# Kernel optimization log

Measured on AMD Instinct MI355X. Metric: run time of the kernel, lower is better.

The kernel has to match this reference:

```python
import jax, jax.numpy as jnp
import numpy as np

SCALE = 0.1
TEMP = 1.0
LN_EPS = 1e-6
NORM_EPS = 1e-12  # torch F.normalize eps


def setup_inputs() -> dict:
    key = jax.random.key(0)
    k1, = jax.random.split(key, 1)
    B, N, D = 8, 2048, 256
    x = jax.random.normal(k1, (B, N, D), dtype=jnp.float32)
    ln_gamma = jnp.ones((D,), dtype=jnp.float32)
    ln_beta = jnp.zeros((D,), dtype=jnp.float32)
    return {"x": x, "ln_gamma": ln_gamma, "ln_beta": ln_beta}


def reference(x, ln_gamma, ln_beta):
    # L2-normalize along feature dim (torch F.normalize, dim=2)
    norm = jnp.sqrt(jnp.sum(x * x, axis=2, keepdims=True))
    xn = x / jnp.maximum(norm, NORM_EPS)
    # self-similarity: [B, N, N]
    sim = jnp.einsum('bnd,bmd->bnm', xn, xn) / TEMP
    # dual_norm: row softmax + column softmax
    sim = jax.nn.softmax(sim, axis=2) + jax.nn.softmax(sim, axis=1)
    x_neg = jnp.einsum('bnm,bmd->bnd', sim, x)
    x = x - SCALE * x_neg
    # LayerNorm(dim), eps=1e-6
    mu = jnp.mean(x, axis=-1, keepdims=True)
    var = jnp.mean((x - mu) ** 2, axis=-1, keepdims=True)
    xhat = (x - mu) * jax.lax.rsqrt(var + LN_EPS)
    return xhat * ln_gamma + ln_beta
```

## Files before the change

### kernel.cpp

```cpp
#include <hip/hip_runtime.h>

namespace {
constexpr int Bv = 8;
constexpr int Nv = 2048;
constexpr int Dv = 256;
constexpr float SCALE = 0.1f;
constexpr float PSCALE = 256.0f;
constexpr float OSC = SCALE / PSCALE;
constexpr float LN_EPS = 1e-6f;
constexpr float NORM_EPS = 1e-12f;
}

typedef unsigned char u8;
typedef unsigned int u32;
typedef __attribute__((ext_vector_type(4))) float f32x4;

__device__ __forceinline__ void gll16(const void* g, void* l) {
    __builtin_amdgcn_global_load_lds(
        (__attribute__((address_space(1))) void*)(uintptr_t)g,
        (__attribute__((address_space(3))) void*)(uintptr_t)l, 16, 0, 0);
}
__device__ __forceinline__ u32 pk4(float a, float b, float c, float d) {
    u32 w = __builtin_amdgcn_cvt_pk_fp8_f32(a, b, 0, false);
    return __builtin_amdgcn_cvt_pk_fp8_f32(c, d, w, true);
}

__global__ __launch_bounds__(512) void k_prepT(const float* __restrict__ x,
                                               u8* __restrict__ xn8,
                                               u8* __restrict__ xT8) {
    __shared__ u8 lt[64][272];
    const int b = blockIdx.x >> 5;
    const int n0 = (blockIdx.x & 31) * 64;
    const int t = threadIdx.x;
    const int r = t >> 3, c0 = (t & 7) * 32;
    const float* xr = x + ((size_t)b * Nv + n0 + r) * Dv + c0;
    float4 v[8];
    float ss = 0.f;
#pragma unroll
    for (int i = 0; i < 8; ++i) {
        v[i] = ((const float4*)xr)[i];
        ss += v[i].x * v[i].x + v[i].y * v[i].y + v[i].z * v[i].z + v[i].w * v[i].w;
    }
#pragma unroll
    for (int m = 1; m < 8; m <<= 1) ss += __shfl_xor(ss, m, 64);
    const float inv = 1.0f / fmaxf(sqrtf(ss), NORM_EPS);
    u32 wn[8];
#pragma unroll
    for (int i = 0; i < 8; ++i) {
        wn[i] = pk4(v[i].x * inv, v[i].y * inv, v[i].z * inv, v[i].w * inv);
        *(u32*)&lt[r][c0 + i * 4] = pk4(v[i].x, v[i].y, v[i].z, v[i].w);
    }
    {
        uint4 o0 = {wn[0], wn[1], wn[2], wn[3]};
        uint4 o1 = {wn[4], wn[5], wn[6], wn[7]};
        u8* xnr = xn8 + ((size_t)b * Nv + n0 + r) * Dv + c0;
        *(uint4*)xnr = o0;
        *(uint4*)(xnr + 16) = o1;
    }
    __syncthreads();
    {
        const int d = t >> 1, h = t & 1;
        u32 w2[8];
#pragma unroll
        for (int q = 0; q < 8; ++q) {
            const int nb = h * 32 + q * 4;
            w2[q] = (u32)lt[nb][d] | ((u32)lt[nb + 1][d] << 8) |
                    ((u32)lt[nb + 2][d] << 16) | ((u32)lt[nb + 3][d] << 24);
        }
        uint4 p0 = {w2[0], w2[1], w2[2], w2[3]};
        uint4 p1 = {w2[4], w2[5], w2[6], w2[7]};
        u8* xtr = xT8 + ((size_t)b * Dv + d) * Nv + n0 + h * 32;
        *(uint4*)xtr = p0;
        *(uint4*)(xtr + 16) = p1;
    }
}

__global__ __launch_bounds__(512, 4) void k_gemm1(const u8* __restrict__ xn8,
                                                  u8* __restrict__ E,
                                                  float* __restrict__ rl) {
    __shared__ u8 Bs[2][128 * 256];
    __shared__ u8 eS[2][128 * 40];
    __shared__ float red[32][4];
    const int wg = blockIdx.x;
    const int b = wg & 7, bi = wg >> 3;
    const int t = threadIdx.x;
    const int wave = t >> 6, lane = t & 63;
    const int wr = wave >> 2, wc = wave & 3;
    const int l15 = lane & 15, kl = lane >> 4;
    const u8* xb = xn8 + (size_t)b * (Nv * Dv);

    auto stageB = [&](int buf, int ch) {
#pragma unroll
        for (int c = 0; c < 4; ++c) {
            const int row = wave * 16 + c * 4 + (lane >> 4);
            const int slot = (lane & 15) ^ (row & 15);
            gll16(xb + (size_t)(ch * 128 + row) * Dv + slot * 16,
                  Bs[buf] + wave * 4096 + c * 1024);
        }
    };
    auto bfrag = [&](const u8* base, int row, int kk) -> long {
        const int slot = kk * 2 + (kl >> 1);
        return *(const long*)(base + row * 256 +
                              ((slot ^ (row & 15)) << 4) + ((kl & 1) << 3));
    };

    const int ch0 = bi >> 2;
    stageB(0, ch0);
    __syncthreads();
    long af[8];
    {
        const int arow = (bi & 3) * 32 + wr * 16 + l15;
#pragma unroll
        for (int kk = 0; kk < 8; ++kk) af[kk] = bfrag(Bs[0], arow, kk);
    }
    float rs[4] = {0.f, 0.f, 0.f, 0.f};
    u8* Eb = E + (size_t)b * Nv * Nv;
    int cur = 0;
    for (int cc = 0; cc < 16; ++cc) {
        const int ch = (ch0 + cc) & 15;
        if (cc < 15) stageB(cur ^ 1, (ch0 + cc + 1) & 15);
        f32x4 acc[2] = {};
#pragma unroll
        for (int kk = 0; kk < 8; ++kk) {
            const long b0 = bfrag(Bs[cur], wc * 32 + l15, kk);
            const long b1 = bfrag(Bs[cur], wc * 32 + 16 + l15, kk);
            acc[0] = __builtin_amdgcn_mfma_f32_16x16x32_fp8_fp8(af[kk], b0, acc[0], 0, 0, 0);
            acc[1] = __builtin_amdgcn_mfma_f32_16x16x32_fp8_fp8(af[kk], b1, acc[1], 0, 0, 0);
        }
#pragma unroll
        for (int j = 0; j < 2; ++j) {
            const int col = wc * 32 + j * 16 + l15;
            const float e0 = __expf(acc[j][0] - 1.0f);
            const float e1 = __expf(acc[j][1] - 1.0f);
            const float e2 = __expf(acc[j][2] - 1.0f);
            const float e3 = __expf(acc[j][3] - 1.0f);
            rs[0] += e0; rs[1] += e1; rs[2] += e2; rs[3] += e3;
            *(u32*)&eS[cur][col * 40 + wr * 16 + kl * 4] = pk4(e0, e1, e2, e3);
        }
        __syncthreads();
        {
            const int c = t >> 2, sg = t & 3;
            *(uint2*)&Eb[(size_t)(ch * 128 + c) * Nv + bi * 32 + sg * 8] =
                *(const uint2*)&eS[cur][c * 40 + sg * 8];
        }
        cur ^= 1;
    }
#pragma unroll
    for (int r = 0; r < 4; ++r) {
        float v = rs[r];
#pragma unroll
        for (int m = 1; m < 16; m <<= 1) v += __shfl_xor(v, m, 64);
        if (l15 == 0) red[wr * 16 + kl * 4 + r][wc] = v;
    }
    __syncthreads();
    if (t < 32)
        rl[b * Nv + bi * 32 + t] =
            PSCALE * __builtin_amdgcn_rcpf(red[t][0] + red[t][1] + red[t][2] + red[t][3]);
}

__global__ __launch_bounds__(512) void k_gemm2ln(const u8* __restrict__ E,
                                                 const float* __restrict__ rl,
                                                 const u8* __restrict__ xT8,
                                                 const float* __restrict__ x,
                                                 const float* __restrict__ gamma,
                                                 const float* __restrict__ beta,
                                                 float* __restrict__ out) {
    __shared__ u8 Bs[2][256 * 128];
    __shared__ u8 Ps[2][32 * 136];
    __shared__ float red[32][8][2];
    const int wg = blockIdx.x;
    const int swz = (wg & 7) * 64 + (wg >> 3);
    const int b = swz >> 6, bi = swz & 63;
    const int t = threadIdx.x;
    const int wave = t >> 6, lane = t & 63;
    const int l15 = lane & 15, kl = lane >> 4;
    const int srow = t >> 4, s16 = t & 15;
    const float* rlb = rl + (size_t)b * Nv;
    const u8* Erow = E + ((size_t)b * Nv + bi * 32 + srow) * Nv + s16 * 8;
    const u8* xtb = xT8 + (size_t)b * 524288;

    auto issueB = [&](int buf, int kt) {
#pragma unroll
        for (int c = 0; c < 4; ++c) {
            const int row = c * 64 + wave * 8 + (lane >> 3);
            const int slot = (lane & 7) ^ (row & 7);
            gll16(xtb + (size_t)row * Nv + kt * 128 + slot * 16,
                  (char*)Bs[buf] + c * 8192 + wave * 1024);
        }
    };
    auto bfragB = [&](const u8* base, int d, int kk) -> long {
        const int s = kk * 2 + (kl >> 1);
        return *(const long*)(base + d * 128 + ((s ^ (d & 7)) << 4) + ((kl & 1) << 3));
    };
    auto afrag = [&](const u8* base, int row, int kk) -> long {
        return *(const long*)(base + row * 136 + kk * 32 + kl * 8);
    };

    const float linv_n = rlb[bi * 32 + srow];
    auto wstore = [&](u8* pbuf, uint2 ev, float4 ra, float4 rb) {
        const u32 o0 = pk4(__builtin_amdgcn_cvt_f32_fp8(ev.x, 0) * (linv_n + ra.x),
                           __builtin_amdgcn_cvt_f32_fp8(ev.x, 1) * (linv_n + ra.y),
                           __builtin_amdgcn_cvt_f32_fp8(ev.x, 2) * (linv_n + ra.z),
                           __builtin_amdgcn_cvt_f32_fp8(ev.x, 3) * (linv_n + ra.w));
        const u32 o1 = pk4(__builtin_amdgcn_cvt_f32_fp8(ev.y, 0) * (linv_n + rb.x),
                           __builtin_amdgcn_cvt_f32_fp8(ev.y, 1) * (linv_n + rb.y),
                           __builtin_amdgcn_cvt_f32_fp8(ev.y, 2) * (linv_n + rb.z),
                           __builtin_amdgcn_cvt_f32_fp8(ev.y, 3) * (linv_n + rb.w));
        uint2 o = {o0, o1};
        *(uint2*)(pbuf + srow * 136 + s16 * 8) = o;
    };

    issueB(0, 0);
    uint2 evB = *(const uint2*)(Erow);
    float4 raB = *(const float4*)&rlb[s16 * 8];
    float4 rbB = *(const float4*)&rlb[s16 * 8 + 4];
    wstore(Ps[0], evB, raB, rbB);
    evB = *(const uint2*)(Erow + 128);
    uint2 evC = *(const uint2*)(Erow + 256);
    raB = *(const float4*)&rlb[128 + s16 * 8];
    rbB = *(const float4*)&rlb[128 + s16 * 8 + 4];
    __syncthreads();

    f32x4 acc[2][2] = {};
    int cur = 0;
    for (int kt = 0; kt < 16; ++kt) {
        if (kt < 15) issueB(cur ^ 1, kt + 1);
#pragma unroll
        for (int kk = 0; kk < 4; ++kk) {
            const long a0 = afrag(Ps[cur], l15, kk);
            const long a1 = afrag(Ps[cur], 16 + l15, kk);
            const long b0 = bfragB(Bs[cur], wave * 32 + l15, kk);
            const long b1 = bfragB(Bs[cur], wave * 32 + 16 + l15, kk);
            acc[0][0] = __builtin_amdgcn_mfma_f32_16x16x32_fp8_fp8(a0, b0, acc[0][0], 0, 0, 0);
            acc[0][1] = __builtin_amdgcn_mfma_f32_16x16x32_fp8_fp8(a0, b1, acc[0][1], 0, 0, 0);
            acc[1][0] = __builtin_amdgcn_mfma_f32_16x16x32_fp8_fp8(a1, b0, acc[1][0], 0, 0, 0);
            acc[1][1] = __builtin_amdgcn_mfma_f32_16x16x32_fp8_fp8(a1, b1, acc[1][1], 0, 0, 0);
        }
        if (kt < 15) {
            wstore(Ps[cur ^ 1], evB, raB, rbB);
            evB = evC;
            if (kt < 14) {
                evC = *(const uint2*)(Erow + (kt + 2) * 128);
                raB = *(const float4*)&rlb[(kt + 1) * 128 + s16 * 8];
                rbB = *(const float4*)&rlb[(kt + 1) * 128 + s16 * 8 + 4];
            }
        }
        __syncthreads();
        cur ^= 1;
    }
    const float* xb = x + ((size_t)b * Nv + bi * 32) * Dv;
    float tv[2][2][4];
#pragma unroll
    for (int i = 0; i < 2; ++i) {
#pragma unroll
        for (int r = 0; r < 4; ++r) {
            const int rr = i * 16 + kl * 4 + r;
            float s1 = 0.f, s2 = 0.f;
#pragma unroll
            for (int j = 0; j < 2; ++j) {
                const int cc = wave * 32 + j * 16 + l15;
                const float v = xb[(size_t)rr * Dv + cc] - OSC * acc[i][j][r];
                tv[i][j][r] = v;
                s1 += v; s2 += v * v;
            }
#pragma unroll
            for (int m = 1; m < 16; m <<= 1) {
                s1 += __shfl_xor(s1, m, 64);
                s2 += __shfl_xor(s2, m, 64);
            }
            if (l15 == 0) { red[rr][wave][0] = s1; red[rr][wave][1] = s2; }
        }
    }
    __syncthreads();
#pragma unroll
    for (int i = 0; i < 2; ++i) {
#pragma unroll
        for (int r = 0; r < 4; ++r) {
            const int rr = i * 16 + kl * 4 + r;
            float s1 = 0.f, s2 = 0.f;
#pragma unroll
            for (int w = 0; w < 8; ++w) { s1 += red[rr][w][0]; s2 += red[rr][w][1]; }
            const float mu = s1 * (1.0f / Dv);
            const float var = s2 * (1.0f / Dv) - mu * mu;
            const float rstd = rsqrtf(var + LN_EPS);
#pragma unroll
            for (int j = 0; j < 2; ++j) {
                const int cc = wave * 32 + j * 16 + l15;
                out[((size_t)b * Nv + bi * 32 + rr) * Dv + cc] =
                    (tv[i][j][r] - mu) * rstd * gamma[cc] + beta[cc];
            }
        }
    }
}

extern "C" void kernel_launch(void* const* d_in, const int* in_sizes, int n_in,
                              void* d_out, int out_size, void* d_ws, size_t ws_size,
                              hipStream_t stream) {
    const float* x = (const float*)d_in[0];
    const float* gamma = (const float*)d_in[1];
    const float* beta = (const float*)d_in[2];
    float* out = (float*)d_out;
    char* ws = (char*)d_ws;
    u8* xn8 = (u8*)ws;
    u8* xT8 = (u8*)(ws + 4194304);
    float* rl = (float*)(ws + 8388608);
    u8* E = (u8*)(ws + 8454144);

    k_prepT<<<Bv * (Nv / 64), 512, 0, stream>>>(x, xn8, xT8);
    k_gemm1<<<Bv * (Nv / 32), 512, 0, stream>>>(xn8, E, rl);
    k_gemm2ln<<<Bv * (Nv / 32), 512, 0, stream>>>(E, rl, xT8, x, gamma, beta, out);
}
```

Before: 66.11 us.

## Replace syncthreads with manual vmcnt waits and deeper prefetch in both GEMM kernels

Both GEMM loops now use explicit s_waitcnt vmcnt/lgkmcnt plus raw s_barrier in place of __syncthreads. This lets global-to-LDS loads for the next two stages stay in flight while the current stage computes. MFMA sections are wrapped in s_setprio to favour matrix issue. The vmcnt counts must exactly match the outstanding load counts, so any miscount risks races or reading stale LDS data.

Measured after the change: 66.74 us. About the same (+1.0%).

```diff
diff --git a/kernel.cpp b/kernel.cpp
--- a/kernel.cpp
+++ b/kernel.cpp
@@ -14,6 +14,11 @@
 typedef unsigned char u8;
 typedef unsigned int u32;
 typedef __attribute__((ext_vector_type(4))) float f32x4;
+
+#define SBAR()   asm volatile("s_barrier" ::: "memory")
+#define WAITV(N) asm volatile("s_waitcnt vmcnt(" #N ")" ::: "memory")
+#define WAITL()  asm volatile("s_waitcnt lgkmcnt(0)" ::: "memory")
+#define CFENCE() asm volatile("" ::: "memory")
 
 __device__ __forceinline__ void gll16(const void* g, void* l) {
     __builtin_amdgcn_global_load_lds(
@@ -88,6 +93,8 @@
     const int wr = wave >> 2, wc = wave & 3;
     const int l15 = lane & 15, kl = lane >> 4;
     const u8* xb = xn8 + (size_t)b * (Nv * Dv);
+    u8* Eb = E + (size_t)b * Nv * Nv;
+    const int sc = t >> 2, sg = t & 3;
 
     auto stageB = [&](int buf, int ch) {
 #pragma unroll
@@ -106,7 +113,9 @@
 
     const int ch0 = bi >> 2;
     stageB(0, ch0);
-    __syncthreads();
+    CFENCE();
+    stageB(1, (ch0 + 1) & 15);
+    WAITV(4); SBAR();
     long af[8];
     {
         const int arow = (bi & 3) * 32 + wr * 16 + l15;
@@ -114,12 +123,10 @@
         for (int kk = 0; kk < 8; ++kk) af[kk] = bfrag(Bs[0], arow, kk);
     }
     float rs[4] = {0.f, 0.f, 0.f, 0.f};
-    u8* Eb = E + (size_t)b * Nv * Nv;
-    int cur = 0;
-    for (int cc = 0; cc < 16; ++cc) {
-        const int ch = (ch0 + cc) & 15;
-        if (cc < 15) stageB(cur ^ 1, (ch0 + cc + 1) & 15);
+
+    auto phaseA = [&](int cur) {
         f32x4 acc[2] = {};
+        __builtin_amdgcn_s_setprio(1);
 #pragma unroll
         for (int kk = 0; kk < 8; ++kk) {
             const long b0 = bfrag(Bs[cur], wc * 32 + l15, kk);
@@ -127,6 +134,7 @@
             acc[0] = __builtin_amdgcn_mfma_f32_16x16x32_fp8_fp8(af[kk], b0, acc[0], 0, 0, 0);
             acc[1] = __builtin_amdgcn_mfma_f32_16x16x32_fp8_fp8(af[kk], b1, acc[1], 0, 0, 0);
         }
+        __builtin_amdgcn_s_setprio(0);
 #pragma unroll
         for (int j = 0; j < 2; ++j) {
             const int col = wc * 32 + j * 16 + l15;
@@ -137,14 +145,27 @@
             rs[0] += e0; rs[1] += e1; rs[2] += e2; rs[3] += e3;
             *(u32*)&eS[cur][col * 40 + wr * 16 + kl * 4] = pk4(e0, e1, e2, e3);
         }
-        __syncthreads();
-        {
-            const int c = t >> 2, sg = t & 3;
-            *(uint2*)&Eb[(size_t)(ch * 128 + c) * Nv + bi * 32 + sg * 8] =
-                *(const uint2*)&eS[cur][c * 40 + sg * 8];
-        }
-        cur ^= 1;
-    }
+    };
+    auto estore = [&](int cur, int ch) {
+        *(uint2*)&Eb[(size_t)(ch * 128 + sc) * Nv + bi * 32 + sg * 8] =
+            *(const uint2*)&eS[cur][sc * 40 + sg * 8];
+    };
+
+    for (int cc = 0; cc < 14; ++cc) {
+        const int cur = cc & 1;
+        phaseA(cur);
+        WAITL(); SBAR();
+        estore(cur, (ch0 + cc) & 15);
+        stageB(cur, (ch0 + cc + 2) & 15);
+        WAITV(5); SBAR();
+    }
+    phaseA(0);
+    WAITL(); SBAR();
+    estore(0, (ch0 + 14) & 15);
+    WAITV(1); SBAR();
+    phaseA(1);
+    WAITL(); SBAR();
+    estore(1, (ch0 + 15) & 15);
 #pragma unroll
     for (int r = 0; r < 4; ++r) {
         float v = rs[r];
@@ -209,22 +230,15 @@
         uint2 o = {o0, o1};
         *(uint2*)(pbuf + srow * 136 + s16 * 8) = o;
     };
-
-    issueB(0, 0);
-    uint2 evB = *(const uint2*)(Erow);
-    float4 raB = *(const float4*)&rlb[s16 * 8];
-    float4 rbB = *(const float4*)&rlb[s16 * 8 + 4];
-    wstore(Ps[0], evB, raB, rbB);
-    evB = *(const uint2*)(Erow + 128);
-    uint2 evC = *(const uint2*)(Erow + 256);
-    raB = *(const float4*)&rlb[128 + s16 * 8];
-    rbB = *(const float4*)&rlb[128 + s16 * 8 + 4];
-    __syncthreads();
+    auto loadgrp = [&](int nk, uint2& ev, float4& ra, float4& rb) {
+        ev = *(const uint2*)(Erow + nk * 128);
+        ra = *(const float4*)&rlb[nk * 128 + s16 * 8];
+        rb = *(const float4*)&rlb[nk * 128 + s16 * 8 + 4];
+    };
 
     f32x4 acc[2][2] = {};
-    int cur = 0;
-    for (int kt = 0; kt < 16; ++kt) {
-        if (kt < 15) issueB(cur ^ 1, kt + 1);
+    auto phaseA = [&](int cur) {
+        __builtin_amdgcn_s_setprio(1);
 #pragma unroll
         for (int kk = 0; kk < 4; ++kk) {
             const long a0 = afrag(Ps[cur], l15, kk);
@@ -236,18 +250,40 @@
             acc[1][0] = __builtin_amdgcn_mfma_f32_16x16x32_fp8_fp8(a1, b0, acc[1][0], 0, 0, 0);
             acc[1][1] = __builtin_amdgcn_mfma_f32_16x16x32_fp8_fp8(a1, b1, acc[1][1], 0, 0, 0);
         }
-        if (kt < 15) {
-            wstore(Ps[cur ^ 1], evB, raB, rbB);
-            evB = evC;
-            if (kt < 14) {
-                evC = *(const uint2*)(Erow + (kt + 2) * 128);
-                raB = *(const float4*)&rlb[(kt + 1) * 128 + s16 * 8];
-                rbB = *(const float4*)&rlb[(kt + 1) * 128 + s16 * 8 + 4];
-            }
-        }
-        __syncthreads();
-        cur ^= 1;
-    }
+        __builtin_amdgcn_s_setprio(0);
+    };
+
+    uint2 evA, evB2;
+    float4 raA, rbA, raB2, rbB2;
+    loadgrp(0, evA, raA, rbA);
+    issueB(0, 0);
+    CFENCE();
+    loadgrp(1, evB2, raB2, rbB2);
+    issueB(1, 1);
+    CFENCE();
+    wstore(Ps[0], evA, raA, rbA);
+    WAITL(); WAITV(7); SBAR();
+
+    for (int kt2 = 0; kt2 < 7; ++kt2) {
+        phaseA(0);
+        wstore(Ps[1], evB2, raB2, rbB2);
+        WAITL(); SBAR();
+        loadgrp(2 * kt2 + 2, evA, raA, rbA);
+        issueB(0, 2 * kt2 + 2);
+        WAITV(7); SBAR();
+        phaseA(1);
+        wstore(Ps[0], evA, raA, rbA);
+        WAITL(); SBAR();
+        loadgrp(2 * kt2 + 3, evB2, raB2, rbB2);
+        issueB(1, 2 * kt2 + 3);
+        WAITV(7); SBAR();
+    }
+    phaseA(0);
+    wstore(Ps[1], evB2, raB2, rbB2);
+    WAITL(); SBAR();
+    WAITV(0); SBAR();
+    phaseA(1);
+
     const float* xb = x + ((size_t)b * Nv + bi * 32) * Dv;
     float tv[2][2][4];
 #pragma unroll
```

## Double row tile to 64 in both GEMM kernels and restructure staging

Applied to the files above, without the earlier changes.

Both GEMM kernels now process 64 rows per workgroup instead of 32, halving the grid to 256 blocks. Each wave computes more MFMA tiles per loaded B fragment, so the same B chunk is reused across twice the rows and fewer passes over xn8 and xT8 are needed. The pipeline changes from prefetching the next buffer before compute to prefetching two stages ahead after compute. The P tile in the second kernel loses its double buffering, and the LayerNorm reduction scratch now reuses that shared buffer. The trade-off is half as many blocks on a 256-CU part and more registers per thread, which may lower occupancy and latency hiding.

New measurement: 77.21 us. 1.17x slower.

```diff
diff --git a/kernel.cpp b/kernel.cpp
--- a/kernel.cpp
+++ b/kernel.cpp
@@ -75,19 +75,20 @@
     }
 }
 
-__global__ __launch_bounds__(512, 4) void k_gemm1(const u8* __restrict__ xn8,
-                                                  u8* __restrict__ E,
-                                                  float* __restrict__ rl) {
+__global__ __launch_bounds__(512) void k_gemm1(const u8* __restrict__ xn8,
+                                               u8* __restrict__ E,
+                                               float* __restrict__ rl) {
     __shared__ u8 Bs[2][128 * 256];
-    __shared__ u8 eS[2][128 * 40];
-    __shared__ float red[32][4];
+    __shared__ u8 eS[128 * 80];
+    __shared__ float red[64][4];
     const int wg = blockIdx.x;
     const int b = wg & 7, bi = wg >> 3;
     const int t = threadIdx.x;
     const int wave = t >> 6, lane = t & 63;
-    const int wr = wave >> 2, wc = wave & 3;
+    const int wrp = wave >> 2, wc = wave & 3;
     const int l15 = lane & 15, kl = lane >> 4;
     const u8* xb = xn8 + (size_t)b * (Nv * Dv);
+    u8* Eb = E + (size_t)b * Nv * Nv;
 
     auto stageB = [&](int buf, int ch) {
 #pragma unroll
@@ -104,57 +105,70 @@
                               ((slot ^ (row & 15)) << 4) + ((kl & 1) << 3));
     };
 
-    const int ch0 = bi >> 2;
+    const int ch0 = bi >> 1;
     stageB(0, ch0);
     __syncthreads();
-    long af[8];
+    long af[2][8];
     {
-        const int arow = (bi & 3) * 32 + wr * 16 + l15;
-#pragma unroll
-        for (int kk = 0; kk < 8; ++kk) af[kk] = bfrag(Bs[0], arow, kk);
-    }
-    float rs[4] = {0.f, 0.f, 0.f, 0.f};
-    u8* Eb = E + (size_t)b * Nv * Nv;
-    int cur = 0;
+#pragma unroll
+        for (int i = 0; i < 2; ++i) {
+            const int arow = (bi & 1) * 64 + wrp * 32 + i * 16 + l15;
+#pragma unroll
+            for (int kk = 0; kk < 8; ++kk) af[i][kk] = bfrag(Bs[0], arow, kk);
+        }
+    }
+    stageB(1, (ch0 + 1) & 15);
+    __syncthreads();
+
+    float rs[2][4] = {};
     for (int cc = 0; cc < 16; ++cc) {
         const int ch = (ch0 + cc) & 15;
-        if (cc < 15) stageB(cur ^ 1, (ch0 + cc + 1) & 15);
-        f32x4 acc[2] = {};
+        const int cur = cc & 1;
+        f32x4 acc[2][2] = {};
 #pragma unroll
         for (int kk = 0; kk < 8; ++kk) {
             const long b0 = bfrag(Bs[cur], wc * 32 + l15, kk);
             const long b1 = bfrag(Bs[cur], wc * 32 + 16 + l15, kk);
-            acc[0] = __builtin_amdgcn_mfma_f32_16x16x32_fp8_fp8(af[kk], b0, acc[0], 0, 0, 0);
-            acc[1] = __builtin_amdgcn_mfma_f32_16x16x32_fp8_fp8(af[kk], b1, acc[1], 0, 0, 0);
-        }
-#pragma unroll
-        for (int j = 0; j < 2; ++j) {
-            const int col = wc * 32 + j * 16 + l15;
-            const float e0 = __expf(acc[j][0] - 1.0f);
-            const float e1 = __expf(acc[j][1] - 1.0f);
-            const float e2 = __expf(acc[j][2] - 1.0f);
-            const float e3 = __expf(acc[j][3] - 1.0f);
-            rs[0] += e0; rs[1] += e1; rs[2] += e2; rs[3] += e3;
-            *(u32*)&eS[cur][col * 40 + wr * 16 + kl * 4] = pk4(e0, e1, e2, e3);
+#pragma unroll
+            for (int i = 0; i < 2; ++i) {
+                acc[i][0] = __builtin_amdgcn_mfma_f32_16x16x32_fp8_fp8(af[i][kk], b0, acc[i][0], 0, 0, 0);
+                acc[i][1] = __builtin_amdgcn_mfma_f32_16x16x32_fp8_fp8(af[i][kk], b1, acc[i][1], 0, 0, 0);
+            }
+        }
+#pragma unroll
+        for (int i = 0; i < 2; ++i) {
+#pragma unroll
+            for (int j = 0; j < 2; ++j) {
+                const int col = wc * 32 + j * 16 + l15;
+                const float e0 = __expf(acc[i][j][0] - 1.0f);
+                const float e1 = __expf(acc[i][j][1] - 1.0f);
+                const float e2 = __expf(acc[i][j][2] - 1.0f);
+                const float e3 = __expf(acc[i][j][3] - 1.0f);
+                rs[i][0] += e0; rs[i][1] += e1; rs[i][2] += e2; rs[i][3] += e3;
+                *(u32*)&eS[col * 80 + wrp * 32 + i * 16 + kl * 4] = pk4(e0, e1, e2, e3);
+            }
         }
         __syncthreads();
         {
-            const int c = t >> 2, sg = t & 3;
-            *(uint2*)&Eb[(size_t)(ch * 128 + c) * Nv + bi * 32 + sg * 8] =
-                *(const uint2*)&eS[cur][c * 40 + sg * 8];
-        }
-        cur ^= 1;
-    }
-#pragma unroll
-    for (int r = 0; r < 4; ++r) {
-        float v = rs[r];
-#pragma unroll
-        for (int m = 1; m < 16; m <<= 1) v += __shfl_xor(v, m, 64);
-        if (l15 == 0) red[wr * 16 + kl * 4 + r][wc] = v;
-    }
-    __syncthreads();
-    if (t < 32)
-        rl[b * Nv + bi * 32 + t] =
+            const int m = t >> 2, q = t & 3;
+            *(uint4*)&Eb[(size_t)(ch * 128 + m) * Nv + bi * 64 + q * 16] =
+                *(const uint4*)&eS[m * 80 + q * 16];
+        }
+        if (cc < 14) stageB(cur, (ch0 + cc + 2) & 15);
+        __syncthreads();
+    }
+#pragma unroll
+    for (int i = 0; i < 2; ++i)
+#pragma unroll
+        for (int r = 0; r < 4; ++r) {
+            float v = rs[i][r];
+#pragma unroll
+            for (int m = 1; m < 16; m <<= 1) v += __shfl_xor(v, m, 64);
+            if (l15 == 0) red[wrp * 32 + i * 16 + kl * 4 + r][wc] = v;
+        }
+    __syncthreads();
+    if (t < 64)
+        rl[b * Nv + bi * 64 + t] =
             PSCALE * __builtin_amdgcn_rcpf(red[t][0] + red[t][1] + red[t][2] + red[t][3]);
 }
 
@@ -166,17 +180,17 @@
                                                  const float* __restrict__ beta,
                                                  float* __restrict__ out) {
     __shared__ u8 Bs[2][256 * 128];
-    __shared__ u8 Ps[2][32 * 136];
-    __shared__ float red[32][8][2];
+    __shared__ u8 Ps[64 * 144];
     const int wg = blockIdx.x;
-    const int swz = (wg & 7) * 64 + (wg >> 3);
-    const int b = swz >> 6, bi = swz & 63;
+    const int swz = (wg & 7) * 32 + (wg >> 3);
+    const int b = swz >> 5, bi = swz & 31;
     const int t = threadIdx.x;
     const int wave = t >> 6, lane = t & 63;
+    const int wrp = wave >> 2, wcol = wave & 3;
     const int l15 = lane & 15, kl = lane >> 4;
-    const int srow = t >> 4, s16 = t & 15;
+    const int srow = t >> 3, s8 = t & 7;
     const float* rlb = rl + (size_t)b * Nv;
-    const u8* Erow = E + ((size_t)b * Nv + bi * 32 + srow) * Nv + s16 * 8;
+    const u8* Erow = E + ((size_t)b * Nv + bi * 64 + srow) * Nv + s8 * 16;
     const u8* xtb = xT8 + (size_t)b * 524288;
 
     auto issueB = [&](int buf, int kt) {
@@ -192,73 +206,87 @@
         const int s = kk * 2 + (kl >> 1);
         return *(const long*)(base + d * 128 + ((s ^ (d & 7)) << 4) + ((kl & 1) << 3));
     };
-    auto afrag = [&](const u8* base, int row, int kk) -> long {
-        return *(const long*)(base + row * 136 + kk * 32 + kl * 8);
-    };
-
-    const float linv_n = rlb[bi * 32 + srow];
-    auto wstore = [&](u8* pbuf, uint2 ev, float4 ra, float4 rb) {
-        const u32 o0 = pk4(__builtin_amdgcn_cvt_f32_fp8(ev.x, 0) * (linv_n + ra.x),
-                           __builtin_amdgcn_cvt_f32_fp8(ev.x, 1) * (linv_n + ra.y),
-                           __builtin_amdgcn_cvt_f32_fp8(ev.x, 2) * (linv_n + ra.z),
-                           __builtin_amdgcn_cvt_f32_fp8(ev.x, 3) * (linv_n + ra.w));
-        const u32 o1 = pk4(__builtin_amdgcn_cvt_f32_fp8(ev.y, 0) * (linv_n + rb.x),
-                           __builtin_amdgcn_cvt_f32_fp8(ev.y, 1) * (linv_n + rb.y),
-                           __builtin_amdgcn_cvt_f32_fp8(ev.y, 2) * (linv_n + rb.z),
-                           __builtin_amdgcn_cvt_f32_fp8(ev.y, 3) * (linv_n + rb.w));
-        uint2 o = {o0, o1};
-        *(uint2*)(pbuf + srow * 136 + s16 * 8) = o;
+
+    const float linv_n = rlb[bi * 64 + srow];
+    auto wstore = [&](uint4 ev, float4 r0, float4 r1, float4 r2, float4 r3) {
+        const u32 o0 = pk4(__builtin_amdgcn_cvt_f32_fp8(ev.x, 0) * (linv_n + r0.x),
+                           __builtin_amdgcn_cvt_f32_fp8(ev.x, 1) * (linv_n + r0.y),
+                           __builtin_amdgcn_cvt_f32_fp8(ev.x, 2) * (linv_n + r0.z),
+                           __builtin_amdgcn_cvt_f32_fp8(ev.x, 3) * (linv_n + r0.w));
+        const u32 o1 = pk4(__builtin_amdgcn_cvt_f32_fp8(ev.y, 0) * (linv_n + r1.x),
+                           __builtin_amdgcn_cvt_f32_fp8(ev.y, 1) * (linv_n + r1.y),
+                           __builtin_amdgcn_cvt_f32_fp8(ev.y, 2) * (linv_n + r1.z),
+                           __builtin_amdgcn_cvt_f32_fp8(ev.y, 3) * (linv_n + r1.w));
+        const u32 o2 = pk4(__builtin_amdgcn_cvt_f32_fp8(ev.z, 0) * (linv_n + r2.x),
+                           __builtin_amdgcn_cvt_f32_fp8(ev.z, 1) * (linv_n + r2.y),
+                           __builtin_amdgcn_cvt_f32_fp8(ev.z, 2) * (linv_n + r2.z),
+                           __builtin_amdgcn_cvt_f32_fp8(ev.z, 3) * (linv_n + r2.w));
+        const u32 o3 = pk4(__builtin_amdgcn_cvt_f32_fp8(ev.w, 0) * (linv_n + r3.x),
+                           __builtin_amdgcn_cvt_f32_fp8(ev.w, 1) * (linv_n + r3.y),
+                           __builtin_amdgcn_cvt_f32_fp8(ev.w, 2) * (linv_n + r3.z),
+                           __builtin_amdgcn_cvt_f32_fp8(ev.w, 3) * (linv_n + r3.w));
+        uint4 o = {o0, o1, o2, o3};
+        *(uint4*)&Ps[srow * 144 + s8 * 16] = o;
     };
 
     issueB(0, 0);
-    uint2 evB = *(const uint2*)(Erow);
-    float4 raB = *(const float4*)&rlb[s16 * 8];
-    float4 rbB = *(const float4*)&rlb[s16 * 8 + 4];
-    wstore(Ps[0], evB, raB, rbB);
-    evB = *(const uint2*)(Erow + 128);
-    uint2 evC = *(const uint2*)(Erow + 256);
-    raB = *(const float4*)&rlb[128 + s16 * 8];
-    rbB = *(const float4*)&rlb[128 + s16 * 8 + 4];
-    __syncthreads();
-
-    f32x4 acc[2][2] = {};
-    int cur = 0;
+    uint4 ev = *(const uint4*)(Erow);
+    float4 q0 = *(const float4*)&rlb[s8 * 16];
+    float4 q1 = *(const float4*)&rlb[s8 * 16 + 4];
+    float4 q2 = *(const float4*)&rlb[s8 * 16 + 8];
+    float4 q3 = *(const float4*)&rlb[s8 * 16 + 12];
+    __syncthreads();
+    wstore(ev, q0, q1, q2, q3);
+    issueB(1, 1);
+    ev = *(const uint4*)(Erow + 128);
+    q0 = *(const float4*)&rlb[128 + s8 * 16];
+    q1 = *(const float4*)&rlb[128 + s8 * 16 + 4];
+    q2 = *(const float4*)&rlb[128 + s8 * 16 + 8];
+    q3 = *(const float4*)&rlb[128 + s8 * 16 + 12];
+    __syncthreads();
+
+    f32x4 acc[2][4] = {};
     for (int kt = 0; kt < 16; ++kt) {
-        if (kt < 15) issueB(cur ^ 1, kt + 1);
+        const u8* bs = Bs[kt & 1];
 #pragma unroll
         for (int kk = 0; kk < 4; ++kk) {
-            const long a0 = afrag(Ps[cur], l15, kk);
-            const long a1 = afrag(Ps[cur], 16 + l15, kk);
-            const long b0 = bfragB(Bs[cur], wave * 32 + l15, kk);
-            const long b1 = bfragB(Bs[cur], wave * 32 + 16 + l15, kk);
-            acc[0][0] = __builtin_amdgcn_mfma_f32_16x16x32_fp8_fp8(a0, b0, acc[0][0], 0, 0, 0);
-            acc[0][1] = __builtin_amdgcn_mfma_f32_16x16x32_fp8_fp8(a0, b1, acc[0][1], 0, 0, 0);
-            acc[1][0] = __builtin_amdgcn_mfma_f32_16x16x32_fp8_fp8(a1, b0, acc[1][0], 0, 0, 0);
-            acc[1][1] = __builtin_amdgcn_mfma_f32_16x16x32_fp8_fp8(a1, b1, acc[1][1], 0, 0, 0);
-        }
+            const long a0 = *(const long*)&Ps[(wrp * 32 + l15) * 144 + kk * 32 + kl * 8];
+            const long a1 = *(const long*)&Ps[(wrp * 32 + 16 + l15) * 144 + kk * 32 + kl * 8];
+#pragma unroll
+            for (int j = 0; j < 4; ++j) {
+                const long bj = bfragB(bs, wcol * 64 + j * 16 + l15, kk);
+                acc[0][j] = __builtin_amdgcn_mfma_f32_16x16x32_fp8_fp8(a0, bj, acc[0][j], 0, 0, 0);
+                acc[1][j] = __builtin_amdgcn_mfma_f32_16x16x32_fp8_fp8(a1, bj, acc[1][j], 0, 0, 0);
+            }
+        }
+        __syncthreads();
         if (kt < 15) {
-            wstore(Ps[cur ^ 1], evB, raB, rbB);
-            evB = evC;
+            wstore(ev, q0, q1, q2, q3);
             if (kt < 14) {
-                evC = *(const uint2*)(Erow + (kt + 2) * 128);
-                raB = *(const float4*)&rlb[(kt + 1) * 128 + s16 * 8];
-                rbB = *(const float4*)&rlb[(kt + 1) * 128 + s16 * 8 + 4];
-            }
-        }
-        __syncthreads();
-        cur ^= 1;
-    }
-    const float* xb = x + ((size_t)b * Nv + bi * 32) * Dv;
-    float tv[2][2][4];
+                issueB(kt & 1, kt + 2);
+                const int k2 = (kt + 2) * 128;
+                ev = *(const uint4*)(Erow + k2);
+                q0 = *(const float4*)&rlb[k2 + s8 * 16];
+                q1 = *(const float4*)&rlb[k2 + s8 * 16 + 4];
+                q2 = *(const float4*)&rlb[k2 + s8 * 16 + 8];
+                q3 = *(const float4*)&rlb[k2 + s8 * 16 + 12];
+            }
+            __syncthreads();
+        }
+    }
+    float (*red)[4][2] = (float (*)[4][2])(void*)Ps;
+    __syncthreads();
+    const float* xb = x + ((size_t)b * Nv + bi * 64) * Dv;
+    float tv[2][4][4];
 #pragma unroll
     for (int i = 0; i < 2; ++i) {
 #pragma unroll
         for (int r = 0; r < 4; ++r) {
-            const int rr = i * 16 + kl * 4 + r;
+            const int rr = wrp * 32 + i * 16 + kl * 4 + r;
             float s1 = 0.f, s2 = 0.f;
 #pragma unroll
-            for (int j = 0; j < 2; ++j) {
-                const int cc = wave * 32 + j * 16 + l15;
+            for (int j = 0; j < 4; ++j) {
+                const int cc = wcol * 64 + j * 16 + l15;
                 const float v = xb[(size_t)rr * Dv + cc] - OSC * acc[i][j][r];
                 tv[i][j][r] = v;
                 s1 += v; s2 += v * v;
@@ -268,7 +296,7 @@
                 s1 += __shfl_xor(s1, m, 64);
                 s2 += __shfl_xor(s2, m, 64);
             }
-            if (l15 == 0) { red[rr][wave][0] = s1; red[rr][wave][1] = s2; }
+            if (l15 == 0) { red[rr][wcol][0] = s1; red[rr][wcol][1] = s2; }
         }
     }
     __syncthreads();
@@ -276,17 +304,16 @@
     for (int i = 0; i < 2; ++i) {
 #pragma unroll
         for (int r = 0; r < 4; ++r) {
-            const int rr = i * 16 + kl * 4 + r;
-            float s1 = 0.f, s2 = 0.f;
-#pragma unroll
-            for (int w = 0; w < 8; ++w) { s1 += red[rr][w][0]; s2 += red[rr][w][1]; }
+            const int rr = wrp * 32 + i * 16 + kl * 4 + r;
+            const float s1 = red[rr][0][0] + red[rr][1][0] + red[rr][2][0] + red[rr][3][0];
+            const float s2 = red[rr][0][1] + red[rr][1][1] + red[rr][2][1] + red[rr][3][1];
             const float mu = s1 * (1.0f / Dv);
             const float var = s2 * (1.0f / Dv) - mu * mu;
             const float rstd = rsqrtf(var + LN_EPS);
 #pragma unroll
-            for (int j = 0; j < 2; ++j) {
-                const int cc = wave * 32 + j * 16 + l15;
-                out[((size_t)b * Nv + bi * 32 + rr) * Dv + cc] =
+            for (int j = 0; j < 4; ++j) {
+                const int cc = wcol * 64 + j * 16 + l15;
+                out[((size_t)b * Nv + bi * 64 + rr) * Dv + cc] =
                     (tv[i][j][r] - mu) * rstd * gamma[cc] + beta[cc];
             }
         }
@@ -307,6 +334,6 @@
     u8* E = (u8*)(ws + 8454144);
 
     k_prepT<<<Bv * (Nv / 64), 512, 0, stream>>>(x, xn8, xT8);
-    k_gemm1<<<Bv * (Nv / 32), 512, 0, stream>>>(xn8, E, rl);
-    k_gemm2ln<<<Bv * (Nv / 32), 512, 0, stream>>>(E, rl, xT8, x, gamma, beta, out);
-}
+    k_gemm1<<<Bv * (Nv / 64), 512, 0, stream>>>(xn8, E, rl);
+    k_gemm2ln<<<Bv * (Nv / 64), 512, 0, stream>>>(E, rl, xT8, x, gamma, beta, out);
+}
```

## Enlarge K/N chunks to 256 and switch both GEMMs to single-buffered LDS

Applied to the files above, without the earlier changes.

Both GEMM kernels now stage 256-row (or 256-column) chunks in one LDS buffer instead of double-buffered 128-wide chunks. Each iteration does twice the MFMA work, and the loop has half as many iterations and barriers. E stores and loads also widen to 16-byte vectors. The cost is that global-to-LDS loads are no longer overlapped with compute, since staging happens between two barriers after the compute phase. The min-blocks-per-CU hint is also dropped from gemm1, which may change occupancy.

After: 71.20 us. +7.7%, slower.

```diff
diff --git a/kernel.cpp b/kernel.cpp
--- a/kernel.cpp
+++ b/kernel.cpp
@@ -75,11 +75,11 @@
     }
 }
 
-__global__ __launch_bounds__(512, 4) void k_gemm1(const u8* __restrict__ xn8,
-                                                  u8* __restrict__ E,
-                                                  float* __restrict__ rl) {
-    __shared__ u8 Bs[2][128 * 256];
-    __shared__ u8 eS[2][128 * 40];
+__global__ __launch_bounds__(512) void k_gemm1(const u8* __restrict__ xn8,
+                                               u8* __restrict__ E,
+                                               float* __restrict__ rl) {
+    __shared__ u8 Bs[256 * 256];
+    __shared__ u8 eS[256 * 40];
     __shared__ float red[32][4];
     const int wg = blockIdx.x;
     const int b = wg & 7, bi = wg >> 3;
@@ -88,62 +88,62 @@
     const int wr = wave >> 2, wc = wave & 3;
     const int l15 = lane & 15, kl = lane >> 4;
     const u8* xb = xn8 + (size_t)b * (Nv * Dv);
-
-    auto stageB = [&](int buf, int ch) {
-#pragma unroll
-        for (int c = 0; c < 4; ++c) {
-            const int row = wave * 16 + c * 4 + (lane >> 4);
+    u8* Eb = E + (size_t)b * Nv * Nv;
+
+    auto stage = [&](int ch) {
+#pragma unroll
+        for (int c = 0; c < 8; ++c) {
+            const int row = wave * 32 + c * 4 + (lane >> 4);
             const int slot = (lane & 15) ^ (row & 15);
-            gll16(xb + (size_t)(ch * 128 + row) * Dv + slot * 16,
-                  Bs[buf] + wave * 4096 + c * 1024);
-        }
-    };
-    auto bfrag = [&](const u8* base, int row, int kk) -> long {
+            gll16(xb + (size_t)(ch * 256 + row) * Dv + slot * 16,
+                  Bs + wave * 8192 + c * 1024);
+        }
+    };
+    auto bfrag = [&](int row, int kk) -> long {
         const int slot = kk * 2 + (kl >> 1);
-        return *(const long*)(base + row * 256 +
+        return *(const long*)(Bs + row * 256 +
                               ((slot ^ (row & 15)) << 4) + ((kl & 1) << 3));
     };
 
-    const int ch0 = bi >> 2;
-    stageB(0, ch0);
+    const int ch0 = bi >> 3;
+    stage(ch0);
     __syncthreads();
     long af[8];
     {
-        const int arow = (bi & 3) * 32 + wr * 16 + l15;
-#pragma unroll
-        for (int kk = 0; kk < 8; ++kk) af[kk] = bfrag(Bs[0], arow, kk);
+        const int arow = (bi & 7) * 32 + wr * 16 + l15;
+#pragma unroll
+        for (int kk = 0; kk < 8; ++kk) af[kk] = bfrag(arow, kk);
     }
     float rs[4] = {0.f, 0.f, 0.f, 0.f};
-    u8* Eb = E + (size_t)b * Nv * Nv;
-    int cur = 0;
-    for (int cc = 0; cc < 16; ++cc) {
-        const int ch = (ch0 + cc) & 15;
-        if (cc < 15) stageB(cur ^ 1, (ch0 + cc + 1) & 15);
-        f32x4 acc[2] = {};
+    for (int cc = 0; cc < 8; ++cc) {
+        const int ch = (ch0 + cc) & 7;
+        f32x4 acc[4] = {};
 #pragma unroll
         for (int kk = 0; kk < 8; ++kk) {
-            const long b0 = bfrag(Bs[cur], wc * 32 + l15, kk);
-            const long b1 = bfrag(Bs[cur], wc * 32 + 16 + l15, kk);
-            acc[0] = __builtin_amdgcn_mfma_f32_16x16x32_fp8_fp8(af[kk], b0, acc[0], 0, 0, 0);
-            acc[1] = __builtin_amdgcn_mfma_f32_16x16x32_fp8_fp8(af[kk], b1, acc[1], 0, 0, 0);
-        }
-#pragma unroll
-        for (int j = 0; j < 2; ++j) {
-            const int col = wc * 32 + j * 16 + l15;
+#pragma unroll
+            for (int j = 0; j < 4; ++j) {
+                const long bj = bfrag(wc * 64 + j * 16 + l15, kk);
+                acc[j] = __builtin_amdgcn_mfma_f32_16x16x32_fp8_fp8(af[kk], bj, acc[j], 0, 0, 0);
+            }
+        }
+#pragma unroll
+        for (int j = 0; j < 4; ++j) {
+            const int col = wc * 64 + j * 16 + l15;
             const float e0 = __expf(acc[j][0] - 1.0f);
             const float e1 = __expf(acc[j][1] - 1.0f);
             const float e2 = __expf(acc[j][2] - 1.0f);
             const float e3 = __expf(acc[j][3] - 1.0f);
             rs[0] += e0; rs[1] += e1; rs[2] += e2; rs[3] += e3;
-            *(u32*)&eS[cur][col * 40 + wr * 16 + kl * 4] = pk4(e0, e1, e2, e3);
+            *(u32*)&eS[col * 40 + wr * 16 + kl * 4] = pk4(e0, e1, e2, e3);
         }
         __syncthreads();
         {
-            const int c = t >> 2, sg = t & 3;
-            *(uint2*)&Eb[(size_t)(ch * 128 + c) * Nv + bi * 32 + sg * 8] =
-                *(const uint2*)&eS[cur][c * 40 + sg * 8];
-        }
-        cur ^= 1;
+            const int c2 = t >> 1, half = t & 1;
+            *(uint4*)&Eb[(size_t)(ch * 256 + c2) * Nv + bi * 32 + half * 16] =
+                *(const uint4*)&eS[c2 * 40 + half * 16];
+        }
+        if (cc < 7) stage((ch0 + cc + 1) & 7);
+        __syncthreads();
     }
 #pragma unroll
     for (int r = 0; r < 4; ++r) {
@@ -165,8 +165,8 @@
                                                  const float* __restrict__ gamma,
                                                  const float* __restrict__ beta,
                                                  float* __restrict__ out) {
-    __shared__ u8 Bs[2][256 * 128];
-    __shared__ u8 Ps[2][32 * 136];
+    __shared__ u8 Bs[256 * 256];
+    __shared__ u8 Ps[32 * 264];
     __shared__ float red[32][8][2];
     const int wg = blockIdx.x;
     const int swz = (wg & 7) * 64 + (wg >> 3);
@@ -176,77 +176,93 @@
     const int l15 = lane & 15, kl = lane >> 4;
     const int srow = t >> 4, s16 = t & 15;
     const float* rlb = rl + (size_t)b * Nv;
-    const u8* Erow = E + ((size_t)b * Nv + bi * 32 + srow) * Nv + s16 * 8;
+    const u8* Erow = E + ((size_t)b * Nv + bi * 32 + srow) * Nv + s16 * 16;
     const u8* xtb = xT8 + (size_t)b * 524288;
 
-    auto issueB = [&](int buf, int kt) {
-#pragma unroll
-        for (int c = 0; c < 4; ++c) {
-            const int row = c * 64 + wave * 8 + (lane >> 3);
-            const int slot = (lane & 7) ^ (row & 7);
-            gll16(xtb + (size_t)row * Nv + kt * 128 + slot * 16,
-                  (char*)Bs[buf] + c * 8192 + wave * 1024);
-        }
-    };
-    auto bfragB = [&](const u8* base, int d, int kk) -> long {
-        const int s = kk * 2 + (kl >> 1);
-        return *(const long*)(base + d * 128 + ((s ^ (d & 7)) << 4) + ((kl & 1) << 3));
-    };
-    auto afrag = [&](const u8* base, int row, int kk) -> long {
-        return *(const long*)(base + row * 136 + kk * 32 + kl * 8);
+    auto stage = [&](int kt) {
+#pragma unroll
+        for (int c = 0; c < 8; ++c) {
+            const int row = wave * 32 + c * 4 + (lane >> 4);
+            const int slot = (lane & 15) ^ (row & 15);
+            gll16(xtb + (size_t)row * Nv + kt * 256 + slot * 16,
+                  Bs + wave * 8192 + c * 1024);
+        }
+    };
+    auto bfragB = [&](int d, int kk) -> long {
+        const int slot = kk * 2 + (kl >> 1);
+        return *(const long*)(Bs + d * 256 +
+                              ((slot ^ (d & 15)) << 4) + ((kl & 1) << 3));
     };
 
     const float linv_n = rlb[bi * 32 + srow];
-    auto wstore = [&](u8* pbuf, uint2 ev, float4 ra, float4 rb) {
-        const u32 o0 = pk4(__builtin_amdgcn_cvt_f32_fp8(ev.x, 0) * (linv_n + ra.x),
-                           __builtin_amdgcn_cvt_f32_fp8(ev.x, 1) * (linv_n + ra.y),
-                           __builtin_amdgcn_cvt_f32_fp8(ev.x, 2) * (linv_n + ra.z),
-                           __builtin_amdgcn_cvt_f32_fp8(ev.x, 3) * (linv_n + ra.w));
-        const u32 o1 = pk4(__builtin_amdgcn_cvt_f32_fp8(ev.y, 0) * (linv_n + rb.x),
-                           __builtin_amdgcn_cvt_f32_fp8(ev.y, 1) * (linv_n + rb.y),
-                           __builtin_amdgcn_cvt_f32_fp8(ev.y, 2) * (linv_n + rb.z),
-                           __builtin_amdgcn_cvt_f32_fp8(ev.y, 3) * (linv_n + rb.w));
-        uint2 o = {o0, o1};
-        *(uint2*)(pbuf + srow * 136 + s16 * 8) = o;
-    };
-
-    issueB(0, 0);
-    uint2 evB = *(const uint2*)(Erow);
-    float4 raB = *(const float4*)&rlb[s16 * 8];
-    float4 rbB = *(const float4*)&rlb[s16 * 8 + 4];
-    wstore(Ps[0], evB, raB, rbB);
-    evB = *(const uint2*)(Erow + 128);
-    uint2 evC = *(const uint2*)(Erow + 256);
-    raB = *(const float4*)&rlb[128 + s16 * 8];
-    rbB = *(const float4*)&rlb[128 + s16 * 8 + 4];
+    auto wstore = [&](uint4 ev, float4 r0, float4 r1, float4 r2, float4 r3) {
+        const u32 o0 = pk4(__builtin_amdgcn_cvt_f32_fp8(ev.x, 0) * (linv_n + r0.x),
+                           __builtin_amdgcn_cvt_f32_fp8(ev.x, 1) * (linv_n + r0.y),
+                           __builtin_amdgcn_cvt_f32_fp8(ev.x, 2) * (linv_n + r0.z),
+                           __builtin_amdgcn_cvt_f32_fp8(ev.x, 3) * (linv_n + r0.w));
+        const u32 o1 = pk4(__builtin_amdgcn_cvt_f32_fp8(ev.y, 0) * (linv_n + r1.x),
+                           __builtin_amdgcn_cvt_f32_fp8(ev.y, 1) * (linv_n + r1.y),
+                           __builtin_amdgcn_cvt_f32_fp8(ev.y, 2) * (linv_n + r1.z),
+                           __builtin_amdgcn_cvt_f32_fp8(ev.y, 3) * (linv_n + r1.w));
+        const u32 o2 = pk4(__builtin_amdgcn_cvt_f32_fp8(ev.z, 0) * (linv_n + r2.x),
+                           __builtin_amdgcn_cvt_f32_fp8(ev.z, 1) * (linv_n + r2.y),
+                           __builtin_amdgcn_cvt_f32_fp8(ev.z, 2) * (linv_n + r2.z),
+                           __builtin_amdgcn_cvt_f32_fp8(ev.z, 3) * (linv_n + r2.w));
+        const u32 o3 = pk4(__builtin_amdgcn_cvt_f32_fp8(ev.w, 0) * (linv_n + r3.x),
+                           __builtin_amdgcn_cvt_f32_fp8(ev.w, 1) * (linv_n + r3.y),
+                           __builtin_amdgcn_cvt_f32_fp8(ev.w, 2) * (linv_n + r3.z),
+                           __builtin_amdgcn_cvt_f32_fp8(ev.w, 3) * (linv_n + r3.w));
+        uint2 lo = {o0, o1}, hi = {o2, o3};
+        *(uint2*)&Ps[srow * 264 + s16 * 16] = lo;
+        *(uint2*)&Ps[srow * 264 + s16 * 16 + 8] = hi;
+    };
+
+    stage(0);
+    uint4 ev = *(const uint4*)(Erow);
+    float4 q0 = *(const float4*)&rlb[s16 * 16];
+    float4 q1 = *(const float4*)&rlb[s16 * 16 + 4];
+    float4 q2 = *(const float4*)&rlb[s16 * 16 + 8];
+    float4 q3 = *(const float4*)&rlb[s16 * 16 + 12];
+    __syncthreads();
+    wstore(ev, q0, q1, q2, q3);
+    ev = *(const uint4*)(Erow + 256);
+    q0 = *(const float4*)&rlb[256 + s16 * 16];
+    q1 = *(const float4*)&rlb[256 + s16 * 16 + 4];
+    q2 = *(const float4*)&rlb[256 + s16 * 16 + 8];
+    q3 = *(const float4*)&rlb[256 + s16 * 16 + 12];
     __syncthreads();
 
     f32x4 acc[2][2] = {};
-    int cur = 0;
-    for (int kt = 0; kt < 16; ++kt) {
-        if (kt < 15) issueB(cur ^ 1, kt + 1);
-#pragma unroll
-        for (int kk = 0; kk < 4; ++kk) {
-            const long a0 = afrag(Ps[cur], l15, kk);
-            const long a1 = afrag(Ps[cur], 16 + l15, kk);
-            const long b0 = bfragB(Bs[cur], wave * 32 + l15, kk);
-            const long b1 = bfragB(Bs[cur], wave * 32 + 16 + l15, kk);
-            acc[0][0] = __builtin_amdgcn_mfma_f32_16x16x32_fp8_fp8(a0, b0, acc[0][0], 0, 0, 0);
-            acc[0][1] = __builtin_amdgcn_mfma_f32_16x16x32_fp8_fp8(a0, b1, acc[0][1], 0, 0, 0);
-            acc[1][0] = __builtin_amdgcn_mfma_f32_16x16x32_fp8_fp8(a1, b0, acc[1][0], 0, 0, 0);
-            acc[1][1] = __builtin_amdgcn_mfma_f32_16x16x32_fp8_fp8(a1, b1, acc[1][1], 0, 0, 0);
-        }
-        if (kt < 15) {
-            wstore(Ps[cur ^ 1], evB, raB, rbB);
-            evB = evC;
-            if (kt < 14) {
-                evC = *(const uint2*)(Erow + (kt + 2) * 128);
-                raB = *(const float4*)&rlb[(kt + 1) * 128 + s16 * 8];
-                rbB = *(const float4*)&rlb[(kt + 1) * 128 + s16 * 8 + 4];
-            }
+    for (int kt = 0; kt < 8; ++kt) {
+        long af2[2][8];
+#pragma unroll
+        for (int i = 0; i < 2; ++i)
+#pragma unroll
+            for (int kk = 0; kk < 8; ++kk)
+                af2[i][kk] = *(const long*)&Ps[(i * 16 + l15) * 264 + kk * 32 + kl * 8];
+#pragma unroll
+        for (int kk = 0; kk < 8; ++kk) {
+            const long b0 = bfragB(wave * 32 + l15, kk);
+            const long b1 = bfragB(wave * 32 + 16 + l15, kk);
+            acc[0][0] = __builtin_amdgcn_mfma_f32_16x16x32_fp8_fp8(af2[0][kk], b0, acc[0][0], 0, 0, 0);
+            acc[0][1] = __builtin_amdgcn_mfma_f32_16x16x32_fp8_fp8(af2[0][kk], b1, acc[0][1], 0, 0, 0);
+            acc[1][0] = __builtin_amdgcn_mfma_f32_16x16x32_fp8_fp8(af2[1][kk], b0, acc[1][0], 0, 0, 0);
+            acc[1][1] = __builtin_amdgcn_mfma_f32_16x16x32_fp8_fp8(af2[1][kk], b1, acc[1][1], 0, 0, 0);
         }
         __syncthreads();
-        cur ^= 1;
+        if (kt < 7) {
+            wstore(ev, q0, q1, q2, q3);
+            if (kt < 6) {
+                const int k2 = (kt + 2) * 256;
+                ev = *(const uint4*)(Erow + k2);
+                q0 = *(const float4*)&rlb[k2 + s16 * 16];
+                q1 = *(const float4*)&rlb[k2 + s16 * 16 + 4];
+                q2 = *(const float4*)&rlb[k2 + s16 * 16 + 8];
+                q3 = *(const float4*)&rlb[k2 + s16 * 16 + 12];
+            }
+            stage(kt + 1);
+            __syncthreads();
+        }
     }
     const float* xb = x + ((size_t)b * Nv + bi * 32) * Dv;
     float tv[2][2][4];
```
